# Performance work log

Hardware: AMD Instinct MI355X
Metric: run time of the kernel (lower is better)

## Reference

```python
import jax, jax.numpy as jnp
import numpy as np

B, N, D, R = 512, 1024, 256, 100


def setup_inputs() -> dict:
    key = jax.random.key(0)
    k1, k2, k3, k4 = jax.random.split(key, 4)
    node_feature = jax.random.normal(k1, (B, N, D), dtype=jnp.float32)
    edge_weight = jax.random.randint(k2, (B, N), 0, 2, dtype=jnp.int32)
    relation_label = jax.random.randint(k3, (B,), 0, R, dtype=jnp.int32)
    # nn.Embedding weight, xavier_uniform-style scale
    limit = np.sqrt(6.0 / (R + D)).astype(np.float32)
    relation_matrix = jax.random.uniform(k4, (R, D), dtype=jnp.float32, minval=-limit, maxval=limit)
    return {
        "node_feature": node_feature,
        "edge_weight": edge_weight,
        "relation_label": relation_label,
        "relation_matrix": relation_matrix,
    }


def reference(node_feature, edge_weight, relation_label, relation_matrix):
    # Training path of entity_mention_select, vectorized over the batch.
    # Per entity b: n = node[b][edge[b]==1]  (gather by nonzero mask)
    #   scores = n @ rel[label_b]      -> [M_b]
    #   w = softmax(scores, axis=0)    -> [M_b]
    #   out = w @ n                    -> [D]
    # Masked softmax over the full N axis is mathematically identical to
    # gathering the nonzero entries first (masked slots get weight 0).
    q = relation_matrix[relation_label]                      # [B, D]
    scores = jnp.einsum("bnd,bd->bn", node_feature, q)       # [B, N]
    neg_inf = jnp.finfo(scores.dtype).min
    scores = jnp.where(edge_weight == 1, scores, neg_inf)
    w = jax.nn.softmax(scores, axis=-1)                       # [B, N]
    out = jnp.einsum("bn,bnd->bd", w, node_feature)           # [B, D]
    return out
```

## Files before the change

### kernel.cpp

```cpp
#include <hip/hip_runtime.h>
#include <hip/hip_bf16.h>
#include <math.h>

#define BATCH 512
#define NROWS 1024
#define DDIM  256
#define NWAVES 16

__global__ __launch_bounds__(1024, 8) void attn_pool_kernel(
    const float* __restrict__ node,
    const int*   __restrict__ edge,
    const int*   __restrict__ label,
    const float* __restrict__ rel,
    float*       __restrict__ out)
{
    const int b    = blockIdx.x;
    const int tid  = threadIdx.x;
    const int lane = tid & 63;
    const int wave = tid >> 6;

    const int lab = label[b];
    const float4 q = *(const float4*)(rel + (size_t)lab * DDIM + lane * 4);

    const float4* nodeb = (const float4*)(node + (size_t)b * NROWS * DDIM);
    const int*    edgeb = edge + (size_t)b * NROWS;

    float  m = -INFINITY;
    float  l = 0.0f;
    float4 o = make_float4(0.f, 0.f, 0.f, 0.f);

    for (int n = wave; n < NROWS; n += 2 * NWAVES) {
        const int n2 = n + NWAVES;
        const int e1 = edgeb[n];
        const int e2 = edgeb[n2];

        float4 x1, x2;
        if (e1 == 1) x1 = nodeb[(size_t)n  * (DDIM / 4) + lane];
        if (e2 == 1) x2 = nodeb[(size_t)n2 * (DDIM / 4) + lane];

        if (e1 == 1) {
            float s = x1.x * q.x + x1.y * q.y + x1.z * q.z + x1.w * q.w;
            #pragma unroll
            for (int off = 32; off > 0; off >>= 1) s += __shfl_xor(s, off);
            const float mnew  = fmaxf(m, s);
            const float scale = __expf(m - mnew);
            const float p     = __expf(s - mnew);
            l = l * scale + p;
            o.x = o.x * scale + p * x1.x;
            o.y = o.y * scale + p * x1.y;
            o.z = o.z * scale + p * x1.z;
            o.w = o.w * scale + p * x1.w;
            m = mnew;
        }
        if (e2 == 1) {
            float s = x2.x * q.x + x2.y * q.y + x2.z * q.z + x2.w * q.w;
            #pragma unroll
            for (int off = 32; off > 0; off >>= 1) s += __shfl_xor(s, off);
            const float mnew  = fmaxf(m, s);
            const float scale = __expf(m - mnew);
            const float p     = __expf(s - mnew);
            l = l * scale + p;
            o.x = o.x * scale + p * x2.x;
            o.y = o.y * scale + p * x2.y;
            o.z = o.z * scale + p * x2.z;
            o.w = o.w * scale + p * x2.w;
            m = mnew;
        }
    }

    __shared__ float s_m[NWAVES];
    __shared__ float s_l[NWAVES];
    __shared__ float s_o[NWAVES][DDIM];

    if (lane == 0) { s_m[wave] = m; s_l[wave] = l; }
    *(float4*)&s_o[wave][lane * 4] = o;
    __syncthreads();

    if (tid < DDIM) {
        float M = -INFINITY;
        #pragma unroll
        for (int w = 0; w < NWAVES; ++w) M = fmaxf(M, s_m[w]);
        float L = 0.f, acc = 0.f;
        #pragma unroll
        for (int w = 0; w < NWAVES; ++w) {
            const float sc = __expf(s_m[w] - M);
            L   += s_l[w] * sc;
            acc += s_o[w][tid] * sc;
        }
        out[(size_t)b * DDIM + tid] = acc / L;
    }
}

extern "C" void kernel_launch(void* const* d_in, const int* in_sizes, int n_in,
                              void* d_out, int out_size, void* d_ws, size_t ws_size,
                              hipStream_t stream) {
    const float* node  = (const float*)d_in[0];
    const int*   edge  = (const int*)  d_in[1];
    const int*   label = (const int*)  d_in[2];
    const float* rel   = (const float*)d_in[3];
    float*       out   = (float*)d_out;

    attn_pool_kernel<<<dim3(BATCH), dim3(1024), 0, stream>>>(node, edge, label, rel, out);
}
```

Before: 632.8 us.

## Compact active rows with ballot and batch eight gathered loads per wave

Each thread loads one edge flag and a wave ballot builds a 64-bit mask of active rows in its contiguous 64-row slice. The wave then walks the set bits, issuing eight independent row loads at once and merging them with a single online-softmax rescale per batch. This skips masked rows without per-row branches, gives more memory-level parallelism, and cuts the exp/rescale work per row. It costs more registers, so launch bounds drop from 8 to 4 waves per SIMD. Load imbalance across waves can also appear, because each wave's active count depends on its own slice.

```diff
diff --git a/kernel.cpp b/kernel.cpp
--- a/kernel.cpp
+++ b/kernel.cpp
@@ -6,8 +6,9 @@
 #define NROWS 1024
 #define DDIM  256
 #define NWAVES 16
+#define RBATCH 8
 
-__global__ __launch_bounds__(1024, 8) void attn_pool_kernel(
+__global__ __launch_bounds__(1024, 4) void attn_pool_kernel(
     const float* __restrict__ node,
     const int*   __restrict__ edge,
     const int*   __restrict__ label,
@@ -23,49 +24,72 @@
     const float4 q = *(const float4*)(rel + (size_t)lab * DDIM + lane * 4);
 
     const float4* nodeb = (const float4*)(node + (size_t)b * NROWS * DDIM);
-    const int*    edgeb = edge + (size_t)b * NROWS;
+
+    const int e = edge[(size_t)b * NROWS + tid];
+    unsigned long long mask = __ballot(e == 1);
+
+    const int rowbase = wave * 64;
 
     float  m = -INFINITY;
     float  l = 0.0f;
     float4 o = make_float4(0.f, 0.f, 0.f, 0.f);
 
-    for (int n = wave; n < NROWS; n += 2 * NWAVES) {
-        const int n2 = n + NWAVES;
-        const int e1 = edgeb[n];
-        const int e2 = edgeb[n2];
+    while (mask) {
+        int rows[RBATCH];
+        #pragma unroll
+        for (int j = 0; j < RBATCH; ++j) {
+            if (mask) {
+                rows[j] = __ffsll((unsigned long long)mask) - 1;
+                mask &= (mask - 1);
+            } else {
+                rows[j] = -1;
+            }
+        }
 
-        float4 x1, x2;
-        if (e1 == 1) x1 = nodeb[(size_t)n  * (DDIM / 4) + lane];
-        if (e2 == 1) x2 = nodeb[(size_t)n2 * (DDIM / 4) + lane];
+        float4 x[RBATCH];
+        #pragma unroll
+        for (int j = 0; j < RBATCH; ++j) {
+            x[j] = make_float4(0.f, 0.f, 0.f, 0.f);
+            if (rows[j] >= 0)
+                x[j] = nodeb[(size_t)(rowbase + rows[j]) * (DDIM / 4) + lane];
+        }
 
-        if (e1 == 1) {
-            float s = x1.x * q.x + x1.y * q.y + x1.z * q.z + x1.w * q.w;
+        float s[RBATCH];
+        #pragma unroll
+        for (int j = 0; j < RBATCH; ++j)
+            s[j] = (rows[j] >= 0)
+                 ? (x[j].x * q.x + x[j].y * q.y + x[j].z * q.z + x[j].w * q.w)
+                 : -INFINITY;
+
+        #pragma unroll
+        for (int off = 32; off > 0; off >>= 1) {
             #pragma unroll
-            for (int off = 32; off > 0; off >>= 1) s += __shfl_xor(s, off);
-            const float mnew  = fmaxf(m, s);
-            const float scale = __expf(m - mnew);
-            const float p     = __expf(s - mnew);
-            l = l * scale + p;
-            o.x = o.x * scale + p * x1.x;
-            o.y = o.y * scale + p * x1.y;
-            o.z = o.z * scale + p * x1.z;
-            o.w = o.w * scale + p * x1.w;
-            m = mnew;
+            for (int j = 0; j < RBATCH; ++j)
+                s[j] += __shfl_xor(s[j], off);
         }
-        if (e2 == 1) {
-            float s = x2.x * q.x + x2.y * q.y + x2.z * q.z + x2.w * q.w;
-            #pragma unroll
-            for (int off = 32; off > 0; off >>= 1) s += __shfl_xor(s, off);
-            const float mnew  = fmaxf(m, s);
-            const float scale = __expf(m - mnew);
-            const float p     = __expf(s - mnew);
-            l = l * scale + p;
-            o.x = o.x * scale + p * x2.x;
-            o.y = o.y * scale + p * x2.y;
-            o.z = o.z * scale + p * x2.z;
-            o.w = o.w * scale + p * x2.w;
-            m = mnew;
+
+        float mnew = m;
+        #pragma unroll
+        for (int j = 0; j < RBATCH; ++j) mnew = fmaxf(mnew, s[j]);
+
+        const float scale = __expf(m - mnew);
+        float p[RBATCH];
+        float psum = 0.f;
+        #pragma unroll
+        for (int j = 0; j < RBATCH; ++j) {
+            p[j] = __expf(s[j] - mnew);
+            psum += p[j];
         }
+        l = l * scale + psum;
+        o.x *= scale; o.y *= scale; o.z *= scale; o.w *= scale;
+        #pragma unroll
+        for (int j = 0; j < RBATCH; ++j) {
+            o.x += p[j] * x[j].x;
+            o.y += p[j] * x[j].y;
+            o.z += p[j] * x[j].z;
+            o.w += p[j] * x[j].w;
+        }
+        m = mnew;
     }
 
     __shared__ float s_m[NWAVES];
```

After: 632.2 us. Within noise of the previous version (-0.1%).
